# Optimization experiments

Hardware: AMD Instinct MI355X
Metric: run time of the kernel (lower is better)

The kernel has to match this reference:

```python
import jax, jax.numpy as jnp
import numpy as np

EPS = 1e-8
CMAP_SHARPNESS = 100.0  # sigmoid sharpness in contact_map_of_m_to_n


def setup_inputs() -> dict:
    key = jax.random.key(0)
    k1, k2, k3, k4 = jax.random.split(key, 4)
    N, M, V, F = 8192, 4096, 2048, 2048
    obj_points = jax.random.normal(k1, (N, 3), jnp.float32)
    sr_points = 0.8 * jax.random.normal(k2, (M, 3), jnp.float32)
    verts = 0.8 * jax.random.normal(k3, (V, 3), jnp.float32)
    faces = jax.random.randint(k4, (F, 3), 0, V)
    tri = verts[faces]                                   # [F,3,3]
    fn = jnp.cross(tri[:, 1] - tri[:, 0], tri[:, 2] - tri[:, 0])
    face_normals = fn / (jnp.linalg.norm(fn, axis=-1, keepdims=True) + EPS)
    return {"obj_points": obj_points, "sr_points": sr_points,
            "verts": verts, "faces": faces, "face_normals": face_normals}


def _ray_triangle_hits(origins, dirs, tri, face_normals):
    """Plane-intersection + barycentric inside test. Returns [F,N] bool hits (t>=0)."""
    v0 = tri[:, 0]                                       # [F,3]
    denom = jnp.einsum('fc,nc->fn', face_normals, dirs)  # [F,N]
    safe = jnp.where(jnp.abs(denom) < EPS, EPS, denom)
    num = (jnp.einsum('fc,fc->f', face_normals, v0)[:, None]
           - jnp.einsum('fc,nc->fn', face_normals, origins))
    t = num / safe                                       # [F,N]
    p = origins[None, :, :] + t[..., None] * dirs[None, :, :]  # [F,N,3]
    inside = jnp.ones(t.shape, dtype=bool)
    for i in range(3):  # fixed 3 triangle edges
        vi = tri[:, i]
        vj = tri[:, (i + 1) % 3]
        c = jnp.cross((vj - vi)[:, None, :], p - vi[:, None, :])  # [F,N,3]
        inside = inside & (jnp.einsum('fnc,fc->fn', c, face_normals) >= 0.0)
    return inside & (t >= 0.0) & (jnp.abs(denom) >= EPS)


def reference(obj_points, sr_points, verts, faces, face_normals):
    # get_NN: brute-force nearest sampled hand point for each object point
    d2 = jnp.sum((obj_points[:, None, :] - sr_points[None, :, :]) ** 2, axis=-1)  # [N,M]
    nn_idx = jnp.argmin(d2, axis=1)                      # [N]
    trg_pts = sr_points[nn_idx]                          # batched_index_select
    ray_dirs = trg_pts - obj_points                      # [N,3]
    tri = verts[faces]                                   # v[f] -> [F,3,3]
    hits = _ray_triangle_hits(obj_points, ray_dirs, tri, face_normals)  # [F,N]
    hit_number = jnp.sum(hits.astype(jnp.int32), axis=0)
    interior_mask = (hit_number % 2) != 0                # [N]
    # torch.norm(trg_pts[mask] - obj_points[mask]) == Frobenius norm over masked rows
    pen_dist = jnp.sqrt(jnp.sum(jnp.where(interior_mask[:, None], ray_dirs, 0.0) ** 2))
    # contact_map_of_m_to_n: per-obj-point contact value from NN distance
    nn_dist = jnp.sqrt(jnp.min(d2, axis=1) + EPS)
    cmap = 1.0 - 2.0 * (jax.nn.sigmoid(CMAP_SHARPNESS * nn_dist) - 0.5)
    return pen_dist, cmap
```

## Files before the change

kernel.cpp:

```cpp
#include <hip/hip_runtime.h>
#include <hip/hip_bf16.h>
#include <math.h>

#define EPSF 1e-8f

constexpr int N_OBJ  = 8192;
constexpr int M_SR   = 4096;
constexpr int N_FACE = 2048;

constexpr size_t OFF_FD   = 2 * N_OBJ * sizeof(float4);
constexpr size_t OFF_GCNT = OFF_FD + N_FACE * 16 * sizeof(float);
constexpr size_t OFF_PEN  = OFF_GCNT + 32ull * N_OBJ * sizeof(int);

__global__ __launch_bounds__(256) void face_setup(
    const float* __restrict__ verts, const int* __restrict__ faces,
    const float* __restrict__ fnorm, float* __restrict__ fd)
{
    int f = blockIdx.x * 256 + threadIdx.x;
    if (f >= N_FACE) return;
    int i0 = faces[3 * f + 0], i1 = faces[3 * f + 1], i2 = faces[3 * f + 2];
    float ax = verts[3 * i0 + 0], ay = verts[3 * i0 + 1], az = verts[3 * i0 + 2];
    float bx = verts[3 * i1 + 0], by = verts[3 * i1 + 1], bz = verts[3 * i1 + 2];
    float cx = verts[3 * i2 + 0], cy = verts[3 * i2 + 1], cz = verts[3 * i2 + 2];
    float fx = fnorm[3 * f + 0], fy = fnorm[3 * f + 1], fz = fnorm[3 * f + 2];
    float nf = fx * ax + fy * ay + fz * az;

    float e0x = bx - ax, e0y = by - ay, e0z = bz - az;
    float g0x = fy * e0z - fz * e0y, g0y = fz * e0x - fx * e0z, g0z = fx * e0y - fy * e0x;
    float h0  = g0x * ax + g0y * ay + g0z * az;
    float e1x = cx - bx, e1y = cy - by, e1z = cz - bz;
    float g1x = fy * e1z - fz * e1y, g1y = fz * e1x - fx * e1z, g1z = fx * e1y - fy * e1x;
    float h1  = g1x * bx + g1y * by + g1z * bz;
    float e2x = ax - cx, e2y = ay - cy, e2z = az - cz;
    float g2x = fy * e2z - fz * e2y, g2y = fz * e2x - fx * e2z, g2z = fx * e2y - fy * e2x;
    float h2  = g2x * cx + g2y * cy + g2z * cz;

    float* o = fd + f * 16;
    o[0] = fx;  o[1] = fy;  o[2] = fz;  o[3] = nf;
    o[4] = g0x; o[5] = g0y; o[6] = g0z; o[7] = h0;
    o[8] = g1x; o[9] = g1y; o[10] = g1z; o[11] = h1;
    o[12] = g2x; o[13] = g2y; o[14] = g2z; o[15] = h2;
}

constexpr int SRTILE = 2048;
constexpr int NN_PPW = 2;
constexpr int NN_PPB = NN_PPW * 4;
constexpr int NN_NBLK = N_OBJ / NN_PPB;

__global__ __launch_bounds__(256) void nn_kernel(
    const float* __restrict__ obj, const float* __restrict__ srp,
    float* __restrict__ out, float4* __restrict__ ptrec)
{
    __shared__ float4 s4[SRTILE];
    const int tid  = threadIdx.x;
    const int w    = tid >> 6;
    const int lane = tid & 63;
    const int pbase = blockIdx.x * NN_PPB + w * NN_PPW;

    float ox[NN_PPW], oy[NN_PPW], oz[NN_PPW], oo[NN_PPW], best[NN_PPW];
    int bi[NN_PPW];
#pragma unroll
    for (int q = 0; q < NN_PPW; ++q) {
        int n = pbase + q;
        ox[q] = obj[3 * n]; oy[q] = obj[3 * n + 1]; oz[q] = obj[3 * n + 2];
        oo[q] = ox[q] * ox[q] + oy[q] * oy[q] + oz[q] * oz[q];
        best[q] = 3.4e38f; bi[q] = 0;
    }

    for (int t0 = 0; t0 < M_SR; t0 += SRTILE) {
        __syncthreads();
        for (int i = tid; i < SRTILE; i += 256) {
            float sx = srp[3 * (t0 + i) + 0];
            float sy = srp[3 * (t0 + i) + 1];
            float sz = srp[3 * (t0 + i) + 2];
            s4[i] = make_float4(sx, sy, sz, sx * sx + sy * sy + sz * sz);
        }
        __syncthreads();
#pragma unroll 4
        for (int j = 0; j < SRTILE / 64; ++j) {
            int s = j * 64 + lane;
            float4 v = s4[s];
#pragma unroll
            for (int q = 0; q < NN_PPW; ++q) {
                float m = v.w - 2.0f * (ox[q] * v.x + oy[q] * v.y + oz[q] * v.z);
                if (m < best[q]) { best[q] = m; bi[q] = t0 + s; }
            }
        }
    }
    for (int off = 1; off < 64; off <<= 1) {
#pragma unroll
        for (int q = 0; q < NN_PPW; ++q) {
            float od = __shfl_xor(best[q], off);
            int   oi = __shfl_xor(bi[q], off);
            if (od < best[q] || (od == best[q] && oi < bi[q])) { best[q] = od; bi[q] = oi; }
        }
    }
    if (lane == 0) {
#pragma unroll
        for (int q = 0; q < NN_PPW; ++q) {
            int n = pbase + q;
            float d2 = best[q] + oo[q];
            float dx = srp[3 * bi[q]] - ox[q];
            float dy = srp[3 * bi[q] + 1] - oy[q];
            float dz = srp[3 * bi[q] + 2] - oz[q];
            ptrec[2 * n]     = make_float4(ox[q], oy[q], oz[q], d2);
            ptrec[2 * n + 1] = make_float4(dx, dy, dz, 0.0f);
            out[1 + n] = 2.0f / (1.0f + expf(100.0f * sqrtf(d2 + EPSF)));
        }
    }
}

constexpr int FK_FS   = 32;
constexpr int FK_PB   = N_OBJ / 256;
constexpr int FK_NBLK = FK_PB * FK_FS;

__global__ __launch_bounds__(256) void face_kernel(
    const float* __restrict__ fd, const float4* __restrict__ ptrec,
    int* __restrict__ gcnt)
{
    const int tid   = threadIdx.x;
    const int fs    = blockIdx.x & (FK_FS - 1);
    const int ptblk = blockIdx.x / FK_FS;
    const int p     = ptblk * 256 + tid;

    float4 r0 = ptrec[2 * p];
    float4 r1 = ptrec[2 * p + 1];
    const float pox = r0.x, poy = r0.y, poz = r0.z;
    const float pdx = r1.x, pdy = r1.y, pdz = r1.z;

    const float* __restrict__ c = fd + (fs * 64) * 16;

    int cnt = 0;
#pragma unroll 4
    for (int j = 0; j < 64; ++j) {
        const float fx  = c[16 * j + 0],  fy  = c[16 * j + 1];
        const float fz  = c[16 * j + 2],  nf  = c[16 * j + 3];
        const float g0x = c[16 * j + 4],  g0y = c[16 * j + 5];
        const float g0z = c[16 * j + 6],  h0  = c[16 * j + 7];
        const float g1x = c[16 * j + 8],  g1y = c[16 * j + 9];
        const float g1z = c[16 * j + 10], h1  = c[16 * j + 11];
        const float g2x = c[16 * j + 12], g2y = c[16 * j + 13];
        const float g2z = c[16 * j + 14], h2  = c[16 * j + 15];

        float den = fx * pdx + fy * pdy + fz * pdz;
        float num = nf - (fx * pox + fy * poy + fz * poz);
        float Px  = den * pox + num * pdx;
        float Py  = den * poy + num * pdy;
        float Pz  = den * poz + num * pdz;
        bool pos = den >= 0.0f;
        bool ok0 = ((g0x * Px + g0y * Py + g0z * Pz - den * h0) >= 0.0f) == pos;
        bool ok1 = ((g1x * Px + g1y * Py + g1z * Pz - den * h1) >= 0.0f) == pos;
        bool ok2 = ((g2x * Px + g2y * Py + g2z * Pz - den * h2) >= 0.0f) == pos;
        bool tok = (num >= 0.0f) == pos;
        bool aok = fabsf(den) >= EPSF;
        cnt += (ok0 & ok1 & ok2 & tok & aok) ? 1 : 0;
    }
    gcnt[fs * N_OBJ + p] = cnt;
}

__global__ __launch_bounds__(256) void finP_kernel(
    const float4* __restrict__ ptrec, const int* __restrict__ gcnt,
    float* __restrict__ pensum)
{
    __shared__ float sc[4];
    const int tid = threadIdx.x;
    const int p   = blockIdx.x * 256 + tid;
    int tot = 0;
#pragma unroll
    for (int s = 0; s < FK_FS; ++s) tot += gcnt[s * N_OBJ + p];
    float v = (tot & 1) ? ptrec[2 * p].w : 0.0f;
    for (int off = 1; off < 64; off <<= 1) v += __shfl_xor(v, off);
    if ((tid & 63) == 0) sc[tid >> 6] = v;
    __syncthreads();
    if (tid == 0) pensum[blockIdx.x] = sc[0] + sc[1] + sc[2] + sc[3];
}

__global__ __launch_bounds__(64) void fin2_kernel(
    const float* __restrict__ pensum, float* __restrict__ out)
{
    const int lane = threadIdx.x;
    float v = (lane < FK_PB) ? pensum[lane] : 0.0f;
    for (int off = 1; off < 64; off <<= 1) v += __shfl_xor(v, off);
    if (lane == 0) out[0] = sqrtf(v);
}

extern "C" void kernel_launch(void* const* d_in, const int* in_sizes, int n_in,
                              void* d_out, int out_size, void* d_ws, size_t ws_size,
                              hipStream_t stream)
{
    const float* obj   = (const float*)d_in[0];
    const float* srp   = (const float*)d_in[1];
    const float* verts = (const float*)d_in[2];
    const int*   faces = (const int*)d_in[3];
    const float* fnorm = (const float*)d_in[4];
    float*       out   = (float*)d_out;

    float4* ptrec  = (float4*)d_ws;
    float*  fd     = (float*)((char*)d_ws + OFF_FD);
    int*    gcnt   = (int*)((char*)d_ws + OFF_GCNT);
    float*  pensum = (float*)((char*)d_ws + OFF_PEN);

    face_setup<<<(N_FACE + 255) / 256, 256, 0, stream>>>(verts, faces, fnorm, fd);
    nn_kernel<<<NN_NBLK, 256, 0, stream>>>(obj, srp, out, ptrec);
    face_kernel<<<FK_NBLK, 256, 0, stream>>>(fd, ptrec, gcnt);
    finP_kernel<<<FK_PB, 256, 0, stream>>>(ptrec, gcnt, pensum);
    fin2_kernel<<<1, 64, 0, stream>>>(pensum, out);
}
```

Before: 45.06 us.

## Split NN search across SR chunks and fuse setup, reduction and final kernels

The nearest-neighbor search is restructured so each thread owns one object point and scans a 128-point slice of the surface set. The per-slice candidates are merged inside the face kernel, which then recomputes the ray direction itself. Face setup is folded into the NN launch, and the final reduction becomes a single 1024-thread kernel that XORs byte-packed hit counts, cutting five launches to three. The NN inner loop now reads sr points from global/cache with uniform addresses rather than from LDS. Every face block redundantly redoes the 32-way candidate merge.

```diff
diff --git a/kernel.cpp b/kernel.cpp
--- a/kernel.cpp
+++ b/kernel.cpp
@@ -8,128 +8,106 @@
 constexpr int M_SR   = 4096;
 constexpr int N_FACE = 2048;
 
-constexpr size_t OFF_FD   = 2 * N_OBJ * sizeof(float4);
-constexpr size_t OFF_GCNT = OFF_FD + N_FACE * 16 * sizeof(float);
-constexpr size_t OFF_PEN  = OFF_GCNT + 32ull * N_OBJ * sizeof(int);
+constexpr size_t OFF_CAND = 128 * 1024;
+constexpr size_t OFF_PEN  = OFF_CAND + 32ull * N_OBJ * sizeof(float2);
+constexpr size_t OFF_GC   = OFF_PEN + N_OBJ * sizeof(float);
 
-__global__ __launch_bounds__(256) void face_setup(
+constexpr int NN_SPLITS   = 32;
+constexpr int SR_PER_SPL  = M_SR / NN_SPLITS;
+constexpr int NN_PTBLK    = N_OBJ / 256;
+constexpr int NN_BLOCKS   = NN_PTBLK * NN_SPLITS;
+constexpr int SETUP_BLKS  = N_FACE / 256;
+
+__global__ __launch_bounds__(256) void k1_nn_setup(
+    const float* __restrict__ obj, const float* __restrict__ srp,
     const float* __restrict__ verts, const int* __restrict__ faces,
-    const float* __restrict__ fnorm, float* __restrict__ fd)
+    const float* __restrict__ fnorm, float* __restrict__ fd,
+    float2* __restrict__ cand)
 {
-    int f = blockIdx.x * 256 + threadIdx.x;
-    if (f >= N_FACE) return;
-    int i0 = faces[3 * f + 0], i1 = faces[3 * f + 1], i2 = faces[3 * f + 2];
-    float ax = verts[3 * i0 + 0], ay = verts[3 * i0 + 1], az = verts[3 * i0 + 2];
-    float bx = verts[3 * i1 + 0], by = verts[3 * i1 + 1], bz = verts[3 * i1 + 2];
-    float cx = verts[3 * i2 + 0], cy = verts[3 * i2 + 1], cz = verts[3 * i2 + 2];
-    float fx = fnorm[3 * f + 0], fy = fnorm[3 * f + 1], fz = fnorm[3 * f + 2];
-    float nf = fx * ax + fy * ay + fz * az;
+    const int b   = blockIdx.x;
+    const int tid = threadIdx.x;
 
-    float e0x = bx - ax, e0y = by - ay, e0z = bz - az;
-    float g0x = fy * e0z - fz * e0y, g0y = fz * e0x - fx * e0z, g0z = fx * e0y - fy * e0x;
-    float h0  = g0x * ax + g0y * ay + g0z * az;
-    float e1x = cx - bx, e1y = cy - by, e1z = cz - bz;
-    float g1x = fy * e1z - fz * e1y, g1y = fz * e1x - fx * e1z, g1z = fx * e1y - fy * e1x;
-    float h1  = g1x * bx + g1y * by + g1z * bz;
-    float e2x = ax - cx, e2y = ay - cy, e2z = az - cz;
-    float g2x = fy * e2z - fz * e2y, g2y = fz * e2x - fx * e2z, g2z = fx * e2y - fy * e2x;
-    float h2  = g2x * cx + g2y * cy + g2z * cz;
+    if (b >= NN_BLOCKS) {
+        int f = (b - NN_BLOCKS) * 256 + tid;
+        int i0 = faces[3 * f + 0], i1 = faces[3 * f + 1], i2 = faces[3 * f + 2];
+        float ax = verts[3 * i0 + 0], ay = verts[3 * i0 + 1], az = verts[3 * i0 + 2];
+        float bx = verts[3 * i1 + 0], by = verts[3 * i1 + 1], bz = verts[3 * i1 + 2];
+        float cx = verts[3 * i2 + 0], cy = verts[3 * i2 + 1], cz = verts[3 * i2 + 2];
+        float fx = fnorm[3 * f + 0], fy = fnorm[3 * f + 1], fz = fnorm[3 * f + 2];
+        float nf = fx * ax + fy * ay + fz * az;
 
-    float* o = fd + f * 16;
-    o[0] = fx;  o[1] = fy;  o[2] = fz;  o[3] = nf;
-    o[4] = g0x; o[5] = g0y; o[6] = g0z; o[7] = h0;
-    o[8] = g1x; o[9] = g1y; o[10] = g1z; o[11] = h1;
-    o[12] = g2x; o[13] = g2y; o[14] = g2z; o[15] = h2;
+        float e0x = bx - ax, e0y = by - ay, e0z = bz - az;
+        float g0x = fy * e0z - fz * e0y, g0y = fz * e0x - fx * e0z, g0z = fx * e0y - fy * e0x;
+        float h0  = g0x * ax + g0y * ay + g0z * az;
+        float e1x = cx - bx, e1y = cy - by, e1z = cz - bz;
+        float g1x = fy * e1z - fz * e1y, g1y = fz * e1x - fx * e1z, g1z = fx * e1y - fy * e1x;
+        float h1  = g1x * bx + g1y * by + g1z * bz;
+        float e2x = ax - cx, e2y = ay - cy, e2z = az - cz;
+        float g2x = fy * e2z - fz * e2y, g2y = fz * e2x - fx * e2z, g2z = fx * e2y - fy * e2x;
+        float h2  = g2x * cx + g2y * cy + g2z * cz;
+
+        float* o = fd + f * 16;
+        o[0] = fx;  o[1] = fy;  o[2] = fz;  o[3] = nf;
+        o[4] = g0x; o[5] = g0y; o[6] = g0z; o[7] = h0;
+        o[8] = g1x; o[9] = g1y; o[10] = g1z; o[11] = h1;
+        o[12] = g2x; o[13] = g2y; o[14] = g2z; o[15] = h2;
+        return;
+    }
+
+    const int sp    = b & (NN_SPLITS - 1);
+    const int ptblk = b / NN_SPLITS;
+    const int p     = ptblk * 256 + tid;
+
+    const float ox = obj[3 * p], oy = obj[3 * p + 1], oz = obj[3 * p + 2];
+    const float* __restrict__ s = srp + 3 * sp * SR_PER_SPL;
+
+    float best = 3.4e38f;
+    int   bi   = 0;
+#pragma unroll 8
+    for (int j = 0; j < SR_PER_SPL; ++j) {
+        float dx = ox - s[3 * j + 0];
+        float dy = oy - s[3 * j + 1];
+        float dz = oz - s[3 * j + 2];
+        float d2 = dx * dx + dy * dy + dz * dz;
+        if (d2 < best) { best = d2; bi = sp * SR_PER_SPL + j; }
+    }
+    cand[sp * N_OBJ + p] = make_float2(best, __int_as_float(bi));
 }
 
-constexpr int SRTILE = 2048;
-constexpr int NN_PPW = 2;
-constexpr int NN_PPB = NN_PPW * 4;
-constexpr int NN_NBLK = N_OBJ / NN_PPB;
+constexpr int FK_SPLITS = 32;
+constexpr int FK_PTBLK  = N_OBJ / 256;
+constexpr int FK_NBLK   = FK_PTBLK * FK_SPLITS;
 
-__global__ __launch_bounds__(256) void nn_kernel(
+__global__ __launch_bounds__(256) void k2_face(
     const float* __restrict__ obj, const float* __restrict__ srp,
-    float* __restrict__ out, float4* __restrict__ ptrec)
+    const float* __restrict__ fd, const float2* __restrict__ cand,
+    float* __restrict__ out, float* __restrict__ pend2,
+    unsigned char* __restrict__ gcnt8)
 {
-    __shared__ float4 s4[SRTILE];
-    const int tid  = threadIdx.x;
-    const int w    = tid >> 6;
-    const int lane = tid & 63;
-    const int pbase = blockIdx.x * NN_PPB + w * NN_PPW;
+    const int tid   = threadIdx.x;
+    const int fs    = blockIdx.x & (FK_SPLITS - 1);
+    const int ptblk = blockIdx.x / FK_SPLITS;
+    const int p     = ptblk * 256 + tid;
 
-    float ox[NN_PPW], oy[NN_PPW], oz[NN_PPW], oo[NN_PPW], best[NN_PPW];
-    int bi[NN_PPW];
+    float best = 3.4e38f;
+    int   bi   = 0;
 #pragma unroll
-    for (int q = 0; q < NN_PPW; ++q) {
-        int n = pbase + q;
-        ox[q] = obj[3 * n]; oy[q] = obj[3 * n + 1]; oz[q] = obj[3 * n + 2];
-        oo[q] = ox[q] * ox[q] + oy[q] * oy[q] + oz[q] * oz[q];
-        best[q] = 3.4e38f; bi[q] = 0;
+    for (int s = 0; s < NN_SPLITS; ++s) {
+        float2 c = cand[s * N_OBJ + p];
+        if (c.x < best) { best = c.x; bi = __float_as_int(c.y); }
     }
 
-    for (int t0 = 0; t0 < M_SR; t0 += SRTILE) {
-        __syncthreads();
-        for (int i = tid; i < SRTILE; i += 256) {
-            float sx = srp[3 * (t0 + i) + 0];
-            float sy = srp[3 * (t0 + i) + 1];
-            float sz = srp[3 * (t0 + i) + 2];
-            s4[i] = make_float4(sx, sy, sz, sx * sx + sy * sy + sz * sz);
-        }
-        __syncthreads();
-#pragma unroll 4
-        for (int j = 0; j < SRTILE / 64; ++j) {
-            int s = j * 64 + lane;
-            float4 v = s4[s];
-#pragma unroll
-            for (int q = 0; q < NN_PPW; ++q) {
-                float m = v.w - 2.0f * (ox[q] * v.x + oy[q] * v.y + oz[q] * v.z);
-                if (m < best[q]) { best[q] = m; bi[q] = t0 + s; }
-            }
-        }
+    const float ox = obj[3 * p], oy = obj[3 * p + 1], oz = obj[3 * p + 2];
+    const float pdx = srp[3 * bi + 0] - ox;
+    const float pdy = srp[3 * bi + 1] - oy;
+    const float pdz = srp[3 * bi + 2] - oz;
+
+    if (fs == 0) {
+        pend2[p] = best;
+        out[1 + p] = 2.0f / (1.0f + expf(100.0f * sqrtf(best + EPSF)));
     }
-    for (int off = 1; off < 64; off <<= 1) {
-#pragma unroll
-        for (int q = 0; q < NN_PPW; ++q) {
-            float od = __shfl_xor(best[q], off);
-            int   oi = __shfl_xor(bi[q], off);
-            if (od < best[q] || (od == best[q] && oi < bi[q])) { best[q] = od; bi[q] = oi; }
-        }
-    }
-    if (lane == 0) {
-#pragma unroll
-        for (int q = 0; q < NN_PPW; ++q) {
-            int n = pbase + q;
-            float d2 = best[q] + oo[q];
-            float dx = srp[3 * bi[q]] - ox[q];
-            float dy = srp[3 * bi[q] + 1] - oy[q];
-            float dz = srp[3 * bi[q] + 2] - oz[q];
-            ptrec[2 * n]     = make_float4(ox[q], oy[q], oz[q], d2);
-            ptrec[2 * n + 1] = make_float4(dx, dy, dz, 0.0f);
-            out[1 + n] = 2.0f / (1.0f + expf(100.0f * sqrtf(d2 + EPSF)));
-        }
-    }
-}
-
-constexpr int FK_FS   = 32;
-constexpr int FK_PB   = N_OBJ / 256;
-constexpr int FK_NBLK = FK_PB * FK_FS;
-
-__global__ __launch_bounds__(256) void face_kernel(
-    const float* __restrict__ fd, const float4* __restrict__ ptrec,
-    int* __restrict__ gcnt)
-{
-    const int tid   = threadIdx.x;
-    const int fs    = blockIdx.x & (FK_FS - 1);
-    const int ptblk = blockIdx.x / FK_FS;
-    const int p     = ptblk * 256 + tid;
-
-    float4 r0 = ptrec[2 * p];
-    float4 r1 = ptrec[2 * p + 1];
-    const float pox = r0.x, poy = r0.y, poz = r0.z;
-    const float pdx = r1.x, pdy = r1.y, pdz = r1.z;
 
     const float* __restrict__ c = fd + (fs * 64) * 16;
-
     int cnt = 0;
 #pragma unroll 4
     for (int j = 0; j < 64; ++j) {
@@ -143,10 +121,10 @@
         const float g2z = c[16 * j + 14], h2  = c[16 * j + 15];
 
         float den = fx * pdx + fy * pdy + fz * pdz;
-        float num = nf - (fx * pox + fy * poy + fz * poz);
-        float Px  = den * pox + num * pdx;
-        float Py  = den * poy + num * pdy;
-        float Pz  = den * poz + num * pdz;
+        float num = nf - (fx * ox + fy * oy + fz * oz);
+        float Px  = den * ox + num * pdx;
+        float Py  = den * oy + num * pdy;
+        float Pz  = den * oz + num * pdz;
         bool pos = den >= 0.0f;
         bool ok0 = ((g0x * Px + g0y * Py + g0z * Pz - den * h0) >= 0.0f) == pos;
         bool ok1 = ((g1x * Px + g1y * Py + g1z * Pz - den * h1) >= 0.0f) == pos;
@@ -155,33 +133,44 @@
         bool aok = fabsf(den) >= EPSF;
         cnt += (ok0 & ok1 & ok2 & tok & aok) ? 1 : 0;
     }
-    gcnt[fs * N_OBJ + p] = cnt;
+    gcnt8[fs * N_OBJ + p] = (unsigned char)cnt;
 }
 
-__global__ __launch_bounds__(256) void finP_kernel(
-    const float4* __restrict__ ptrec, const int* __restrict__ gcnt,
-    float* __restrict__ pensum)
+__global__ __launch_bounds__(1024) void k3_fin(
+    const float* __restrict__ pend2, const unsigned char* __restrict__ gcnt8,
+    float* __restrict__ out)
 {
-    __shared__ float sc[4];
-    const int tid = threadIdx.x;
-    const int p   = blockIdx.x * 256 + tid;
-    int tot = 0;
+    __shared__ float wsum[16];
+    const int t  = threadIdx.x;
+    const int p0 = t * 8;
+
+    unsigned int xlo = 0, xhi = 0;
 #pragma unroll
-    for (int s = 0; s < FK_FS; ++s) tot += gcnt[s * N_OBJ + p];
-    float v = (tot & 1) ? ptrec[2 * p].w : 0.0f;
-    for (int off = 1; off < 64; off <<= 1) v += __shfl_xor(v, off);
-    if ((tid & 63) == 0) sc[tid >> 6] = v;
+    for (int fs = 0; fs < FK_SPLITS; ++fs) {
+        uint2 v = *(const uint2*)(gcnt8 + fs * N_OBJ + p0);
+        xlo ^= v.x; xhi ^= v.y;
+    }
+    float4 a = *(const float4*)(pend2 + p0);
+    float4 b = *(const float4*)(pend2 + p0 + 4);
+    float s = 0.0f;
+    if (xlo & 0x1u)        s += a.x;
+    if (xlo & 0x100u)      s += a.y;
+    if (xlo & 0x10000u)    s += a.z;
+    if (xlo & 0x1000000u)  s += a.w;
+    if (xhi & 0x1u)        s += b.x;
+    if (xhi & 0x100u)      s += b.y;
+    if (xhi & 0x10000u)    s += b.z;
+    if (xhi & 0x1000000u)  s += b.w;
+
+    for (int off = 1; off < 64; off <<= 1) s += __shfl_xor(s, off);
+    if ((t & 63) == 0) wsum[t >> 6] = s;
     __syncthreads();
-    if (tid == 0) pensum[blockIdx.x] = sc[0] + sc[1] + sc[2] + sc[3];
-}
-
-__global__ __launch_bounds__(64) void fin2_kernel(
-    const float* __restrict__ pensum, float* __restrict__ out)
-{
-    const int lane = threadIdx.x;
-    float v = (lane < FK_PB) ? pensum[lane] : 0.0f;
-    for (int off = 1; off < 64; off <<= 1) v += __shfl_xor(v, off);
-    if (lane == 0) out[0] = sqrtf(v);
+    if (t == 0) {
+        float tot = 0.0f;
+#pragma unroll
+        for (int k = 0; k < 16; ++k) tot += wsum[k];
+        out[0] = sqrtf(tot);
+    }
 }
 
 extern "C" void kernel_launch(void* const* d_in, const int* in_sizes, int n_in,
@@ -195,14 +184,12 @@
     const float* fnorm = (const float*)d_in[4];
     float*       out   = (float*)d_out;
 
-    float4* ptrec  = (float4*)d_ws;
-    float*  fd     = (float*)((char*)d_ws + OFF_FD);
-    int*    gcnt   = (int*)((char*)d_ws + OFF_GCNT);
-    float*  pensum = (float*)((char*)d_ws + OFF_PEN);
+    float*         fd    = (float*)d_ws;
+    float2*        cand  = (float2*)((char*)d_ws + OFF_CAND);
+    float*         pend2 = (float*)((char*)d_ws + OFF_PEN);
+    unsigned char* gcnt8 = (unsigned char*)((char*)d_ws + OFF_GC);
 
-    face_setup<<<(N_FACE + 255) / 256, 256, 0, stream>>>(verts, faces, fnorm, fd);
-    nn_kernel<<<NN_NBLK, 256, 0, stream>>>(obj, srp, out, ptrec);
-    face_kernel<<<FK_NBLK, 256, 0, stream>>>(fd, ptrec, gcnt);
-    finP_kernel<<<FK_PB, 256, 0, stream>>>(ptrec, gcnt, pensum);
-    fin2_kernel<<<1, 64, 0, stream>>>(pensum, out);
+    k1_nn_setup<<<NN_BLOCKS + SETUP_BLKS, 256, 0, stream>>>(obj, srp, verts, faces, fnorm, fd, cand);
+    k2_face<<<FK_NBLK, 256, 0, stream>>>(obj, srp, fd, cand, out, pend2, gcnt8);
+    k3_fin<<<1, 1024, 0, stream>>>(pend2, gcnt8, out);
 }
```

New measurement: 49.83 us. +10.6%, slower.
